# Kernel tuning notes

Hardware: AMD Instinct MI355X
Metric: run time of the kernel (lower is better)

## Reference

```python
import jax, jax.numpy as jnp
import numpy as np

B, NP1, D = 32, 2001, 512   # batch, 1 verb node + 2000 regions, embedding size
R, NUM_ROLES = 6, 190
NUM_VERBS, VOCAB = 504, 2001


def setup_inputs() -> dict:
    key = jax.random.key(0)
    ks = jax.random.split(key, 10)
    s = lambda fan_in: 1.0 / np.sqrt(fan_in)
    return {
        "vert_states": jax.random.normal(ks[0], (B, NP1, D), jnp.float32),
        "roles": jax.random.uniform(ks[1], (R, NUM_ROLES), jnp.float32),
        "Wr": jax.random.normal(ks[2], (D, NUM_ROLES), jnp.float32) * s(NUM_ROLES),
        "br": jax.random.normal(ks[3], (D,), jnp.float32) * s(NUM_ROLES),
        "Wa": jax.random.normal(ks[4], (1, 2 * D), jnp.float32) * s(2 * D),
        "ba": jax.random.normal(ks[5], (1,), jnp.float32) * s(2 * D),
        "Wv": jax.random.normal(ks[6], (NUM_VERBS, D), jnp.float32) * s(D),
        "bv": jax.random.normal(ks[7], (NUM_VERBS,), jnp.float32) * s(D),
        "Wl": jax.random.normal(ks[8], (VOCAB, D), jnp.float32) * s(D),
        "bl": jax.random.normal(ks[9], (VOCAB,), jnp.float32) * s(D),
    }


def reference(vert_states, roles, Wr, br, Wa, ba, Wv, bv, Wl, bl):
    # verb head: ReLU -> Linear on the verb node (node 0)
    verb_predict = jax.nn.relu(vert_states[:, 0]) @ Wv.T + bv              # [B, num_verbs]

    # role embeddings: Linear(num_roles -> D) on role one-hots
    role_emb = roles @ Wr.T + br                                           # [R, D]

    regions = vert_states[:, 1:]                                           # [B, N, D]
    # role_att Linear(2D -> 1) on concat(role_emb, region) decomposes exactly:
    Wa_role, Wa_vert = Wa[:, :D], Wa[:, D:]
    s_role = role_emb @ Wa_role.T                                          # [R, 1]
    s_vert = regions @ Wa_vert.T                                           # [B, N, 1]
    scores = jnp.tanh(s_role[None, :, None, 0] + s_vert[:, None, :, 0] + ba)  # [B, R, N]
    att = jax.nn.log_softmax(scores, axis=-1)                              # over regions

    # attention-weighted sum over regions (avoids [B,R,N,D] materialization)
    label_embed = jnp.einsum("brn,bnd->brd", att, regions)                 # [B, R, D]

    role_label_predict = jax.nn.relu(label_embed) @ Wl.T + bl              # [B, R, vocab]
    return verb_predict, role_label_predict
```

## Files before the change

### kernel.cpp

```cpp
#include <hip/hip_runtime.h>
#include <math.h>

#define B_      32
#define NP1     2001
#define D_      512
#define R_      6
#define NROLES  190
#define NVERBS  504
#define VOCAB   2001
#define NREG    2000

#define NSPLIT  32
#define CHUNK   64
#define PSTRIDE 3592
#define NUQ     16
#define WS_U    8
#define WS_PART 3048
#define WS_AB   (3048 + 3678208)
#define WS_WLB  (WS_AB + 49152)

typedef __attribute__((ext_vector_type(8))) short  short8v;
typedef __attribute__((ext_vector_type(8))) unsigned short ushort8v;
typedef __attribute__((ext_vector_type(4))) float  f32x4;

__device__ __forceinline__ float fast_tanh(float x) {
    float e = exp2f(x * 2.885390082f);
    return 1.0f - 2.0f * __builtin_amdgcn_rcpf(e + 1.0f);
}
__device__ __forceinline__ float fast_exp(float x) {
    return exp2f(x * 1.442695041f);
}
__device__ __forceinline__ unsigned short f2bf(float f) {
    unsigned u = __float_as_uint(f);
    return (unsigned short)((u + 0x7FFFu + ((u >> 16) & 1u)) >> 16);
}

__device__ __forceinline__ float wave_sum(float v) {
    int x;
    x = __builtin_amdgcn_update_dpp(0, __float_as_int(v), 0xB1, 0xF, 0xF, true);
    v += __int_as_float(x);
    x = __builtin_amdgcn_update_dpp(0, __float_as_int(v), 0x4E, 0xF, 0xF, true);
    v += __int_as_float(x);
    x = __builtin_amdgcn_update_dpp(0, __float_as_int(v), 0x124, 0xF, 0xF, true);
    v += __int_as_float(x);
    x = __builtin_amdgcn_update_dpp(0, __float_as_int(v), 0x128, 0xF, 0xF, true);
    v += __int_as_float(x);
    x = __builtin_amdgcn_ds_swizzle(__float_as_int(v), 0x401F);
    v += __int_as_float(x);
    v += __shfl_xor(v, 32, 64);
    return v;
}

__device__ __forceinline__ void gload_lds16(const float* g, float* l) {
    __builtin_amdgcn_global_load_lds(
        (const __attribute__((address_space(1))) void*)g,
        (__attribute__((address_space(3))) void*)l, 16, 0, 0);
}

__global__ __launch_bounds__(256) void k0a_upart(
    const float* __restrict__ Wr, const float* __restrict__ Wa,
    float* __restrict__ ws_u) {
    const int q = blockIdx.x;
    const int k = threadIdx.x;
    if (k >= NROLES) return;
    float s = 0.f;
    const int d0 = q * 32;
    #pragma unroll 8
    for (int d = 0; d < 32; ++d)
        s += Wr[(size_t)(d0 + d) * NROLES + k] * Wa[d0 + d];
    ws_u[q * NROLES + k] = s;
}

__global__ __launch_bounds__(256, 4) void k1_main(
    const float* __restrict__ vs, const float* __restrict__ Wa,
    const float* __restrict__ roles, const float* __restrict__ br,
    const float* __restrict__ ba, const float* __restrict__ ws_u,
    float* __restrict__ part) {
    const int b     = blockIdx.x / NSPLIT;
    const int split = blockIdx.x % NSPLIT;
    const int tid   = threadIdx.x;
    const int lane  = tid & 63;
    const int w     = tid >> 6;

    __shared__ __align__(16) float smem[4 * 2 * 1024];
    __shared__ float lse_[4][R_];
    float* ring = smem + w * 2048;

    const float4 wvA = *reinterpret_cast<const float4*>(Wa + D_ + lane * 4);
    const float4 wvB = *reinterpret_cast<const float4*>(Wa + D_ + 256 + lane * 4);

    const float* base = vs + (size_t)b * (NP1 * D_) + D_;
    const int n0 = split * CHUNK;
    const int nrows = min(n0 + CHUNK, NREG) - n0;
    const int cnt = (nrows - w + 3) >> 2;
    const int npairs = cnt >> 1;

    #pragma unroll
    for (int k = 0; k < 2; ++k) {
        const float* g0 = base + (size_t)(n0 + w + 8 * k) * D_ + lane * 4;
        float* s0 = ring + k * 1024;
        gload_lds16(g0, s0);
        gload_lds16(g0 + 256, s0 + 256);
        const float* g1 = g0 + 4 * D_;
        gload_lds16(g1, s0 + 512);
        gload_lds16(g1 + 256, s0 + 768);
    }
    asm volatile("" ::: "memory");

    float sr[R_];
    {
        float pr[R_] = {0.f, 0.f, 0.f, 0.f, 0.f, 0.f};
        #pragma unroll
        for (int i = 0; i < 3; ++i) {
            const int k = lane + i * 64;
            if (k < NROLES) {
                float u = 0.f;
                #pragma unroll
                for (int q = 0; q < NUQ; ++q) u += ws_u[q * NROLES + k];
                #pragma unroll
                for (int r = 0; r < R_; ++r) pr[r] += roles[r * NROLES + k] * u;
            }
        }
        float c0 = 0.f;
        #pragma unroll
        for (int i = 0; i < 8; ++i) c0 += Wa[lane + i * 64] * br[lane + i * 64];
        c0 = wave_sum(c0) + ba[0];
        #pragma unroll
        for (int r = 0; r < R_; ++r) sr[r] = wave_sum(pr[r]) + c0;
    }

    float acc[R_][8];
    float rsum[8];
    float sume[R_];
    #pragma unroll
    for (int r = 0; r < R_; ++r) {
        sume[r] = 0.f;
        #pragma unroll
        for (int j = 0; j < 8; ++j) acc[r][j] = 0.f;
    }
    #pragma unroll
    for (int j = 0; j < 8; ++j) rsum[j] = 0.f;

    asm volatile("" ::: "memory");

    int st = 2;
    for (int p = 0; p < npairs; ++p) {
        const int rem = npairs - p;
        if (rem > 1) asm volatile("s_waitcnt vmcnt(4)" ::: "memory");
        else         asm volatile("s_waitcnt vmcnt(0)" ::: "memory");

        const float* l0 = ring + (p & 1) * 1024;
        float4 x0A = *reinterpret_cast<const float4*>(l0 + lane * 4);
        float4 x0B = *reinterpret_cast<const float4*>(l0 + 256 + lane * 4);
        float4 x1A = *reinterpret_cast<const float4*>(l0 + 512 + lane * 4);
        float4 x1B = *reinterpret_cast<const float4*>(l0 + 768 + lane * 4);
        float d0 = x0A.x*wvA.x + x0A.y*wvA.y + x0A.z*wvA.z + x0A.w*wvA.w
                 + x0B.x*wvB.x + x0B.y*wvB.y + x0B.z*wvB.z + x0B.w*wvB.w;
        float d1 = x1A.x*wvA.x + x1A.y*wvA.y + x1A.z*wvA.z + x1A.w*wvA.w
                 + x1B.x*wvB.x + x1B.y*wvB.y + x1B.z*wvB.z + x1B.w*wvB.w;
        if (st < npairs) {
            const float* g0 = base + (size_t)(n0 + w + 8 * st) * D_ + lane * 4;
            float* s0 = ring + (st & 1) * 1024;
            gload_lds16(g0, s0);
            gload_lds16(g0 + 256, s0 + 256);
            const float* g1 = g0 + 4 * D_;
            gload_lds16(g1, s0 + 512);
            gload_lds16(g1 + 256, s0 + 768);
            ++st;
        }
        d0 = wave_sum(d0);
        d1 = wave_sum(d1);
        float xs0[8] = {x0A.x,x0A.y,x0A.z,x0A.w,x0B.x,x0B.y,x0B.z,x0B.w};
        float xs1[8] = {x1A.x,x1A.y,x1A.z,x1A.w,x1B.x,x1B.y,x1B.z,x1B.w};
        #pragma unroll
        for (int r = 0; r < R_; ++r) {
            float t0 = fast_tanh(sr[r] + d0);
            float t1 = fast_tanh(sr[r] + d1);
            sume[r] += fast_exp(t0) + fast_exp(t1);
            #pragma unroll
            for (int j = 0; j < 8; ++j) acc[r][j] += t0 * xs0[j] + t1 * xs1[j];
        }
        #pragma unroll
        for (int j = 0; j < 8; ++j) rsum[j] += xs0[j] + xs1[j];
    }

    __syncthreads();
    float* ls = smem;
    for (int ww = 0; ww < 4; ++ww) {
        if (w == ww) {
            #pragma unroll
            for (int j = 0; j < 8; ++j) {
                const int dd = (j < 4) ? (lane * 4 + j) : (256 + lane * 4 + (j - 4));
                if (ww == 0) {
                    #pragma unroll
                    for (int r = 0; r < R_; ++r) ls[r * D_ + dd] = acc[r][j];
                    ls[6 * D_ + dd] = rsum[j];
                } else {
                    #pragma unroll
                    for (int r = 0; r < R_; ++r) ls[r * D_ + dd] += acc[r][j];
                    ls[6 * D_ + dd] += rsum[j];
                }
            }
            if (lane == 0) {
                #pragma unroll
                for (int r = 0; r < R_; ++r) lse_[ww][r] = sume[r];
            }
        }
        __syncthreads();
    }
    float* dst = part + (size_t)(b * NSPLIT + split) * PSTRIDE;
    for (int i = tid; i < 3584 / 4; i += 256)
        reinterpret_cast<float4*>(dst)[i] = reinterpret_cast<const float4*>(ls)[i];
    if (tid < R_)
        dst[3584 + tid] = lse_[0][tid] + lse_[1][tid] + lse_[2][tid] + lse_[3][tid];
}

__global__ __launch_bounds__(256) void k2_multi(
    const float* __restrict__ part, unsigned short* __restrict__ AB,
    const float* __restrict__ Wl, unsigned short* __restrict__ Wlb,
    const float* __restrict__ vs, const float* __restrict__ Wv,
    const float* __restrict__ bv, float* __restrict__ out_verb) {
    const int bid = blockIdx.x;
    const int t = threadIdx.x;
    if (bid < 256) {
        const int b = bid >> 3;
        const int chunk = bid & 7;
        const int dl = t & 63;
        const int qg = t >> 6;
        const int d = chunk * 64 + dl;
        const float* pb = part + (size_t)b * NSPLIT * PSTRIDE;

        float s[7] = {0.f, 0.f, 0.f, 0.f, 0.f, 0.f, 0.f};
        for (int q = qg * 8; q < qg * 8 + 8; ++q) {
            const float* p = pb + (size_t)q * PSTRIDE;
            #pragma unroll
            for (int r = 0; r < R_; ++r) s[r] += p[r * D_ + d];
            s[6] += p[6 * D_ + d];
        }
        __shared__ float red[4][7][64];
        #pragma unroll
        for (int i = 0; i < 7; ++i) red[qg][i][dl] = s[i];
        __shared__ float lse_s[R_];
        if (t < R_) {
            float se = 0.f;
            for (int q = 0; q < NSPLIT; ++q) se += pb[(size_t)q * PSTRIDE + 3584 + t];
            lse_s[t] = logf(se);
        }
        __syncthreads();
        if (t < 64) {
            float rs = red[0][6][dl] + red[1][6][dl] + red[2][6][dl] + red[3][6][dl];
            #pragma unroll
            for (int r = 0; r < R_; ++r) {
                float sw = red[0][r][dl] + red[1][r][dl] + red[2][r][dl] + red[3][r][dl];
                AB[(size_t)(b * R_ + r) * D_ + d] = f2bf(fmaxf(sw - lse_s[r] * rs, 0.f));
            }
        }
    } else if (bid < 256 + 512) {
        const int ci = bid - 256;
        const int idx = ci * 2048 + t * 8;
        const int row = idx >> 9;
        const int col = idx & 511;
        ushort8v o;
        if (row < VOCAB) {
            float4 a = *reinterpret_cast<const float4*>(Wl + (size_t)row * D_ + col);
            float4 b = *reinterpret_cast<const float4*>(Wl + (size_t)row * D_ + col + 4);
            o[0] = f2bf(a.x); o[1] = f2bf(a.y); o[2] = f2bf(a.z); o[3] = f2bf(a.w);
            o[4] = f2bf(b.x); o[5] = f2bf(b.y); o[6] = f2bf(b.z); o[7] = f2bf(b.w);
        } else {
            o = (ushort8v)0;
        }
        *reinterpret_cast<ushort8v*>(Wlb + idx) = o;
    } else {
        const int q = bid - (256 + 512);
        const int b = q >> 1;
        const int g = q & 1;
        __shared__ __align__(16) float a_s[D_];
        float2 x = reinterpret_cast<const float2*>(vs + (size_t)b * (NP1 * D_))[t];
        reinterpret_cast<float2*>(a_s)[t] = make_float2(fmaxf(x.x, 0.f), fmaxf(x.y, 0.f));
        __syncthreads();
        const int v = g * 252 + t;
        if (t < 252 && v < NVERBS) {
            const float* wrow = Wv + (size_t)v * D_;
            float s = 0.f;
            #pragma unroll 4
            for (int k = 0; k < D_; k += 4) {
                float4 w4 = *reinterpret_cast<const float4*>(wrow + k);
                s += a_s[k] * w4.x + a_s[k + 1] * w4.y + a_s[k + 2] * w4.z + a_s[k + 3] * w4.w;
            }
            out_verb[b * NVERBS + v] = s + bv[v];
        }
    }
}

__global__ __launch_bounds__(256) void k3_mfma(
    const unsigned short* __restrict__ AB, const unsigned short* __restrict__ Wlb,
    const float* __restrict__ bl, float* __restrict__ out_role) {
    const int t    = threadIdx.x;
    const int lane = t & 63;
    const int wid  = t >> 6;
    const int wt   = blockIdx.x * 4 + wid;
    const int mt   = wt >> 5;
    const int vt   = wt & 31;
    const int m0   = mt * 16;
    const int v0   = vt * 64;
    const int rc   = lane & 15;
    const int kg   = lane >> 4;

    const unsigned short* arow = AB + (size_t)(m0 + rc) * D_ + kg * 8;
    f32x4 acc0 = {0.f, 0.f, 0.f, 0.f}, acc1 = {0.f, 0.f, 0.f, 0.f};
    f32x4 acc2 = {0.f, 0.f, 0.f, 0.f}, acc3 = {0.f, 0.f, 0.f, 0.f};

    #pragma unroll 4
    for (int ks = 0; ks < 16; ++ks) {
        const int kb = ks * 32;
        short8v af = *reinterpret_cast<const short8v*>(arow + kb);
        const unsigned short* wb = Wlb + (size_t)(v0 + rc) * D_ + kg * 8 + kb;
        short8v b0 = *reinterpret_cast<const short8v*>(wb);
        short8v b1 = *reinterpret_cast<const short8v*>(wb + 16 * D_);
        short8v b2 = *reinterpret_cast<const short8v*>(wb + 32 * D_);
        short8v b3 = *reinterpret_cast<const short8v*>(wb + 48 * D_);
        acc0 = __builtin_amdgcn_mfma_f32_16x16x32_bf16(af, b0, acc0, 0, 0, 0);
        acc1 = __builtin_amdgcn_mfma_f32_16x16x32_bf16(af, b1, acc1, 0, 0, 0);
        acc2 = __builtin_amdgcn_mfma_f32_16x16x32_bf16(af, b2, acc2, 0, 0, 0);
        acc3 = __builtin_amdgcn_mfma_f32_16x16x32_bf16(af, b3, acc3, 0, 0, 0);
    }
    f32x4 accs[4] = {acc0, acc1, acc2, acc3};
    #pragma unroll
    for (int f = 0; f < 4; ++f) {
        const int v = v0 + f * 16 + rc;
        if (v < VOCAB) {
            const float bb = bl[v];
            #pragma unroll
            for (int j = 0; j < 4; ++j) {
                const int m = m0 + kg * 4 + j;
                out_role[(size_t)m * VOCAB + v] = accs[f][j] + bb;
            }
        }
    }
}

extern "C" void kernel_launch(void* const* d_in, const int* in_sizes, int n_in,
                              void* d_out, int out_size, void* d_ws, size_t ws_size,
                              hipStream_t stream) {
    const float* vs    = (const float*)d_in[0];
    const float* roles = (const float*)d_in[1];
    const float* Wr    = (const float*)d_in[2];
    const float* br    = (const float*)d_in[3];
    const float* Wa    = (const float*)d_in[4];
    const float* ba    = (const float*)d_in[5];
    const float* Wv    = (const float*)d_in[6];
    const float* bv    = (const float*)d_in[7];
    const float* Wl    = (const float*)d_in[8];
    const float* bl    = (const float*)d_in[9];

    float* out_verb = (float*)d_out;
    float* out_role = (float*)d_out + B_ * NVERBS;
    float* ws       = (float*)d_ws;
    unsigned short* AB  = (unsigned short*)(ws + WS_AB);
    unsigned short* Wlb = (unsigned short*)(ws + WS_WLB);

    k0a_upart<<<dim3(NUQ), dim3(256), 0, stream>>>(Wr, Wa, ws + WS_U);
    k1_main<<<dim3(B_ * NSPLIT), dim3(256), 0, stream>>>(vs, Wa, roles, br, ba,
                                                         ws + WS_U, ws + WS_PART);
    k2_multi<<<dim3(256 + 512 + 64), dim3(256), 0, stream>>>(ws + WS_PART, AB, Wl, Wlb,
                                                             vs, Wv, bv, out_verb);
    k3_mfma<<<dim3(96), dim3(256), 0, stream>>>(AB, Wlb, bl, out_role);
}
```

Measured before the change: 72.43 us.

## Move Wl conversion and verb head before main kernel; split MFMA blocks to one wave

The Wl-to-bf16 conversion and the verb-head GEMV move out of the post-reduction kernel into the first kernel alongside the role projection. The reduction kernel now only does the partial-sum reduction, which shortens the critical path between the main pass and the final GEMM. The MFMA kernel is relaunched with one wave per block (384 blocks of 64 threads) instead of four waves per block, spreading the work over more CUs. The extra work in the first kernel may lengthen it, and k1_main still has to wait for it to finish.

```diff
diff --git a/kernel.cpp b/kernel.cpp
--- a/kernel.cpp
+++ b/kernel.cpp
@@ -57,18 +57,58 @@
         (__attribute__((address_space(3))) void*)l, 16, 0, 0);
 }
 
-__global__ __launch_bounds__(256) void k0a_upart(
+__global__ __launch_bounds__(256) void k0_multi(
     const float* __restrict__ Wr, const float* __restrict__ Wa,
-    float* __restrict__ ws_u) {
-    const int q = blockIdx.x;
-    const int k = threadIdx.x;
-    if (k >= NROLES) return;
-    float s = 0.f;
-    const int d0 = q * 32;
-    #pragma unroll 8
-    for (int d = 0; d < 32; ++d)
-        s += Wr[(size_t)(d0 + d) * NROLES + k] * Wa[d0 + d];
-    ws_u[q * NROLES + k] = s;
+    float* __restrict__ ws_u,
+    const float* __restrict__ Wl, unsigned short* __restrict__ Wlb,
+    const float* __restrict__ vs, const float* __restrict__ Wv,
+    const float* __restrict__ bv, float* __restrict__ out_verb) {
+    const int bid = blockIdx.x;
+    const int t = threadIdx.x;
+    if (bid < NUQ) {
+        const int k = t;
+        if (k >= NROLES) return;
+        float s = 0.f;
+        const int d0 = bid * 32;
+        #pragma unroll 8
+        for (int d = 0; d < 32; ++d)
+            s += Wr[(size_t)(d0 + d) * NROLES + k] * Wa[d0 + d];
+        ws_u[bid * NROLES + k] = s;
+    } else if (bid < NUQ + 512) {
+        const int ci = bid - NUQ;
+        const int idx = ci * 2048 + t * 8;
+        const int row = idx >> 9;
+        const int col = idx & 511;
+        ushort8v o;
+        if (row < VOCAB) {
+            float4 a = *reinterpret_cast<const float4*>(Wl + (size_t)row * D_ + col);
+            float4 b = *reinterpret_cast<const float4*>(Wl + (size_t)row * D_ + col + 4);
+            o[0] = f2bf(a.x); o[1] = f2bf(a.y); o[2] = f2bf(a.z); o[3] = f2bf(a.w);
+            o[4] = f2bf(b.x); o[5] = f2bf(b.y); o[6] = f2bf(b.z); o[7] = f2bf(b.w);
+        } else {
+            o = (ushort8v)0;
+        }
+        *reinterpret_cast<ushort8v*>(Wlb + idx) = o;
+    } else {
+        const int q = bid - (NUQ + 512);
+        const int b = q >> 1;
+        const int g = q & 1;
+        __shared__ __align__(16) float a_s[D_];
+        float2 x = reinterpret_cast<const float2*>(vs + (size_t)b * (NP1 * D_))[t];
+        reinterpret_cast<float2*>(a_s)[t] = make_float2(fmaxf(x.x, 0.f), fmaxf(x.y, 0.f));
+        __syncthreads();
+        const int v = g * 252 + t;
+        if (t < 252 && v < NVERBS) {
+            const float* wrow = Wv + (size_t)v * D_;
+            float s = 0.f;
+            #pragma unroll 4
+            for (int k = 0; k < D_; k += 4) {
+                float4 w4 = *reinterpret_cast<const float4*>(wrow + k);
+                s += a_s[k] * w4.x + a_s[k + 1] * w4.y + a_s[k + 2] * w4.z + a_s[k + 3] * w4.w;
+            }
+            out_verb[b * NVERBS + v] = s + bv[v];
+        }
+    }
 }
 
 __global__ __launch_bounds__(256, 4) void k1_main(
@@ -215,90 +255,49 @@
         dst[3584 + tid] = lse_[0][tid] + lse_[1][tid] + lse_[2][tid] + lse_[3][tid];
 }
 
-__global__ __launch_bounds__(256) void k2_multi(
-    const float* __restrict__ part, unsigned short* __restrict__ AB,
-    const float* __restrict__ Wl, unsigned short* __restrict__ Wlb,
-    const float* __restrict__ vs, const float* __restrict__ Wv,
-    const float* __restrict__ bv, float* __restrict__ out_verb) {
+__global__ __launch_bounds__(256) void k2_reduce(
+    const float* __restrict__ part, unsigned short* __restrict__ AB) {
     const int bid = blockIdx.x;
     const int t = threadIdx.x;
-    if (bid < 256) {
-        const int b = bid >> 3;
-        const int chunk = bid & 7;
-        const int dl = t & 63;
-        const int qg = t >> 6;
-        const int d = chunk * 64 + dl;
-        const float* pb = part + (size_t)b * NSPLIT * PSTRIDE;
-
-        float s[7] = {0.f, 0.f, 0.f, 0.f, 0.f, 0.f, 0.f};
-        for (int q = qg * 8; q < qg * 8 + 8; ++q) {
-            const float* p = pb + (size_t)q * PSTRIDE;
-            #pragma unroll
-            for (int r = 0; r < R_; ++r) s[r] += p[r * D_ + d];
-            s[6] += p[6 * D_ + d];
-        }
-        __shared__ float red[4][7][64];
-        #pragma unroll
-        for (int i = 0; i < 7; ++i) red[qg][i][dl] = s[i];
-        __shared__ float lse_s[R_];
-        if (t < R_) {
-            float se = 0.f;
-            for (int q = 0; q < NSPLIT; ++q) se += pb[(size_t)q * PSTRIDE + 3584 + t];
-            lse_s[t] = logf(se);
-        }
-        __syncthreads();
-        if (t < 64) {
-            float rs = red[0][6][dl] + red[1][6][dl] + red[2][6][dl] + red[3][6][dl];
-            #pragma unroll
-            for (int r = 0; r < R_; ++r) {
-                float sw = red[0][r][dl] + red[1][r][dl] + red[2][r][dl] + red[3][r][dl];
-                AB[(size_t)(b * R_ + r) * D_ + d] = f2bf(fmaxf(sw - lse_s[r] * rs, 0.f));
-            }
-        }
-    } else if (bid < 256 + 512) {
-        const int ci = bid - 256;
-        const int idx = ci * 2048 + t * 8;
-        const int row = idx >> 9;
-        const int col = idx & 511;
-        ushort8v o;
-        if (row < VOCAB) {
-            float4 a = *reinterpret_cast<const float4*>(Wl + (size_t)row * D_ + col);
-            float4 b = *reinterpret_cast<const float4*>(Wl + (size_t)row * D_ + col + 4);
-            o[0] = f2bf(a.x); o[1] = f2bf(a.y); o[2] = f2bf(a.z); o[3] = f2bf(a.w);
-            o[4] = f2bf(b.x); o[5] = f2bf(b.y); o[6] = f2bf(b.z); o[7] = f2bf(b.w);
-        } else {
-            o = (ushort8v)0;
-        }
-        *reinterpret_cast<ushort8v*>(Wlb + idx) = o;
-    } else {
-        const int q = bid - (256 + 512);
-        const int b = q >> 1;
-        const int g = q & 1;
-        __shared__ __align__(16) float a_s[D_];
-        float2 x = reinterpret_cast<const float2*>(vs + (size_t)b * (NP1 * D_))[t];
-        reinterpret_cast<float2*>(a_s)[t] = make_float2(fmaxf(x.x, 0.f), fmaxf(x.y, 0.f));
-        __syncthreads();
-        const int v = g * 252 + t;
-        if (t < 252 && v < NVERBS) {
-            const float* wrow = Wv + (size_t)v * D_;
-            float s = 0.f;
-            #pragma unroll 4
-            for (int k = 0; k < D_; k += 4) {
-                float4 w4 = *reinterpret_cast<const float4*>(wrow + k);
-                s += a_s[k] * w4.x + a_s[k + 1] * w4.y + a_s[k + 2] * w4.z + a_s[k + 3] * w4.w;
-            }
-            out_verb[b * NVERBS + v] = s + bv[v];
-        }
-    }
-}
-
-__global__ __launch_bounds__(256) void k3_mfma(
+    const int b = bid >> 3;
+    const int chunk = bid & 7;
+    const int dl = t & 63;
+    const int qg = t >> 6;
+    const int d = chunk * 64 + dl;
+    const float* pb = part + (size_t)b * NSPLIT * PSTRIDE;
+
+    float s[7] = {0.f, 0.f, 0.f, 0.f, 0.f, 0.f, 0.f};
+    for (int q = qg * 8; q < qg * 8 + 8; ++q) {
+        const float* p = pb + (size_t)q * PSTRIDE;
+        #pragma unroll
+        for (int r = 0; r < R_; ++r) s[r] += p[r * D_ + d];
+        s[6] += p[6 * D_ + d];
+    }
+    __shared__ float red[4][7][64];
+    #pragma unroll
+    for (int i = 0; i < 7; ++i) red[qg][i][dl] = s[i];
+    __shared__ float lse_s[R_];
+    if (t < R_) {
+        float se = 0.f;
+        for (int q = 0; q < NSPLIT; ++q) se += pb[(size_t)q * PSTRIDE + 3584 + t];
+        lse_s[t] = logf(se);
+    }
+    __syncthreads();
+    if (t < 64) {
+        float rs = red[0][6][dl] + red[1][6][dl] + red[2][6][dl] + red[3][6][dl];
+        #pragma unroll
+        for (int r = 0; r < R_; ++r) {
+            float sw = red[0][r][dl] + red[1][r][dl] + red[2][r][dl] + red[3][r][dl];
+            AB[(size_t)(b * R_ + r) * D_ + d] = f2bf(fmaxf(sw - lse_s[r] * rs, 0.f));
+        }
+    }
+}
+
+__global__ __launch_bounds__(64) void k3_mfma(
     const unsigned short* __restrict__ AB, const unsigned short* __restrict__ Wlb,
     const float* __restrict__ bl, float* __restrict__ out_role) {
-    const int t    = threadIdx.x;
-    const int lane = t & 63;
-    const int wid  = t >> 6;
-    const int wt   = blockIdx.x * 4 + wid;
+    const int lane = threadIdx.x;
+    const int wt   = blockIdx.x;
     const int mt   = wt >> 5;
     const int vt   = wt & 31;
     const int m0   = mt * 16;
@@ -359,10 +358,10 @@
     unsigned short* AB  = (unsigned short*)(ws + WS_AB);
     unsigned short* Wlb = (unsigned short*)(ws + WS_WLB);
 
-    k0a_upart<<<dim3(NUQ), dim3(256), 0, stream>>>(Wr, Wa, ws + WS_U);
+    k0_multi<<<dim3(NUQ + 512 + 64), dim3(256), 0, stream>>>(Wr, Wa, ws + WS_U,
+                                                             Wl, Wlb, vs, Wv, bv, out_verb);
     k1_main<<<dim3(B_ * NSPLIT), dim3(256), 0, stream>>>(vs, Wa, roles, br, ba,
                                                          ws + WS_U, ws + WS_PART);
-    k2_multi<<<dim3(256 + 512 + 64), dim3(256), 0, stream>>>(ws + WS_PART, AB, Wl, Wlb,
-                                                             vs, Wv, bv, out_verb);
-    k3_mfma<<<dim3(96), dim3(256), 0, stream>>>(AB, Wlb, bl, out_role);
-}
+    k2_reduce<<<dim3(256), dim3(256), 0, stream>>>(ws + WS_PART, AB);
+    k3_mfma<<<dim3(384), dim3(64), 0, stream>>>(AB, Wlb, bl, out_role);
+}
```

New measurement: 67.59 us. 6.7% less time.
